# Kernel tuning notes

Measured on AMD Instinct MI355X. Metric: run time of the kernel, lower is better.

Reference implementation:

```python
import jax, jax.numpy as jnp
import numpy as np

B, S, E = 2, 2048, 1024          # batch, seq, emb_size
H, D = 16, 64                     # heads, head_dim
NE, K = 8, 2                      # num_experts, top_k


def setup_inputs() -> dict:
    key = jax.random.key(0)
    ks = jax.random.split(key, 12)
    w = lambda k, shape: jax.random.normal(k, shape, jnp.float32) * 0.02
    return {
        "x": jax.random.normal(ks[0], (B, S, E), jnp.float32),
        "q_w": w(ks[1], (E, E)), "q_b": jnp.zeros((E,), jnp.float32),
        "k_w": w(ks[2], (E, E)), "k_b": jnp.zeros((E,), jnp.float32),
        "v_w": w(ks[3], (E, E)), "v_b": jnp.zeros((E,), jnp.float32),
        "gate_w": w(ks[4], (NE, E)), "gate_b": jnp.zeros((NE,), jnp.float32),
        "expert_w": w(ks[5], (NE, E, E)), "expert_b": jnp.zeros((NE, E), jnp.float32),
        "ffn_w": w(ks[6], (E, E)), "ffn_b": jnp.zeros((E,), jnp.float32),
    }


def _rope_cos_sin(seq_len, dim):
    inv_freq = 1.0 / (10000.0 ** (jnp.arange(0, dim, 2, dtype=jnp.float32) / dim))
    freqs = jnp.outer(jnp.arange(seq_len, dtype=jnp.float32), inv_freq)  # [S, D/2]
    emb = jnp.concatenate([freqs, freqs], axis=-1)                        # [S, D]
    return jnp.cos(emb), jnp.sin(emb)


def _rotate_half(x):
    x1, x2 = jnp.split(x, 2, axis=-1)
    return jnp.concatenate([-x2, x1], axis=-1)


def reference(x, q_w, q_b, k_w, k_b, v_w, v_b, gate_w, gate_b, expert_w, expert_b, ffn_w, ffn_b):
    b, s, _ = x.shape
    q = (x @ q_w.T + q_b).reshape(b, s, H, D)
    k = (x @ k_w.T + k_b).reshape(b, s, H, D)
    v = (x @ v_w.T + v_b).reshape(b, s, H, D)

    cos, sin = _rope_cos_sin(s, D)          # [S, D]
    cos = cos[None, :, None, :]
    sin = sin[None, :, None, :]
    q = q * cos + _rotate_half(q) * sin
    k = k * cos + _rotate_half(k) * sin

    # full (memory-efficient-style) attention, scale 1/sqrt(D)
    scores = jnp.einsum('bqhd,bkhd->bhqk', q, k) / jnp.sqrt(jnp.float32(D))
    attn = jax.nn.softmax(scores, axis=-1)
    attn_out = jnp.einsum('bhqk,bkhd->bqhd', attn, v).reshape(b, s, E)

    # MoE: dense-compute all experts, gather top-k, weighted combine
    gates = jax.nn.softmax(attn_out @ gate_w.T + gate_b, axis=-1)        # [B,S,NE]
    top_gates, top_idx = jax.lax.top_k(gates, K)                          # [B,S,K]
    # Linear per expert: y = x W^T + b,  expert_w: [NE, out, in]
    expert_outputs = jnp.einsum('bsi,noi->bsno', attn_out, expert_w) + expert_b  # [B,S,NE,E]
    sel = jnp.take_along_axis(expert_outputs, top_idx[..., None], axis=2)        # [B,S,K,E]
    moe_out = jnp.einsum('bsk,bskh->bsh', top_gates, sel)                        # [B,S,E]

    # dropout is identity at inference; ffn + residual
    return moe_out @ ffn_w.T + ffn_b + x
```

## Files before the change

### kernel.cpp

```cpp
#include <hip/hip_runtime.h>
#include <hip/hip_bf16.h>

#define B_ 2
#define S_ 2048
#define E_ 1024
#define H_ 16
#define D_ 64
#define NE_ 8
#define TOKENS (B_*S_)
#define QSCALE 0.18033688011112043f

typedef __attribute__((ext_vector_type(8))) short bf16x8;
typedef __attribute__((ext_vector_type(4))) float f32x4;
typedef unsigned short u16;
typedef unsigned int u32;

#if __has_builtin(__builtin_amdgcn_exp2f)
#define EXP2(x) __builtin_amdgcn_exp2f(x)
#else
#define EXP2(x) exp2f(x)
#endif

__device__ __forceinline__ u16 f2bf(float f) {
    u32 u = __float_as_uint(f);
    u32 r = u + 0x7fffu + ((u >> 16) & 1u);
    return (u16)(r >> 16);
}
__device__ __forceinline__ float bf2f(u16 h) {
    return __uint_as_float(((u32)h) << 16);
}
__device__ __forceinline__ void gl2lds16(const void* g, void* l) {
    __builtin_amdgcn_global_load_lds(
        (__attribute__((address_space(1))) void*)(g),
        (__attribute__((address_space(3))) void*)(l), 16, 0, 0);
}
#define MFMA16(a,b,c) __builtin_amdgcn_mfma_f32_16x16x32_bf16(a,b,c,0,0,0)

__global__ void cvt_all_k(
    const float* __restrict__ x,  const float* __restrict__ qw,
    const float* __restrict__ kw, const float* __restrict__ vw,
    const float* __restrict__ fw, const float* __restrict__ ew,
    u16* __restrict__ xh,  u16* __restrict__ qwh, u16* __restrict__ kwh,
    u16* __restrict__ vwh, u16* __restrict__ fwh, u16* __restrict__ ewh,
    float2* __restrict__ tab)
{
    const int blk = blockIdx.x;
    if (blk < 256) {
        const int idx = blk * 256 + threadIdx.x;
        const int s = idx >> 5, d1 = idx & 31;
        const float inv = exp2f(-(float)d1 * 0.41524101186091903f);
        float sn, cs;
        sincosf((float)s * inv, &sn, &cs);
        tab[idx] = make_float2(cs, sn);
        return;
    }
    const int b2 = blk - 256;
    const float* s; u16* d; int off;
    if (b2 < 4096)      { s = x;  d = xh;  off = b2; }
    else if (b2 < 5120) { s = qw; d = qwh; off = b2 - 4096; }
    else if (b2 < 6144) { s = kw; d = kwh; off = b2 - 5120; }
    else if (b2 < 7168) { s = vw; d = vwh; off = b2 - 6144; }
    else if (b2 < 8192) { s = fw; d = fwh; off = b2 - 7168; }
    else                { s = ew; d = ewh; off = b2 - 8192; }
    const size_t i = (size_t)off * 256 + threadIdx.x;
    const float4 v = *(const float4*)(s + i * 4);
    ushort4 H = {f2bf(v.x), f2bf(v.y), f2bf(v.z), f2bf(v.w)};
    *(ushort4*)(d + i * 4) = H;
}

__global__ __launch_bounds__(256,3) void gemm_qkv(
    const u16* __restrict__ Ah,
    const u16* __restrict__ qwh, const u16* __restrict__ kwh,
    const u16* __restrict__ vwh,
    const float* __restrict__ q_b, const float* __restrict__ k_b,
    const float* __restrict__ v_b,
    const float2* __restrict__ tab,
    u16* __restrict__ Qhb, u16* __restrict__ Khb, u16* __restrict__ Vtb)
{
    __shared__ __align__(16) u16 sA[2][128*32], sB[2][128*32];
    const int lin = blockIdx.x + (blockIdx.y << 3) + (blockIdx.z << 8);
    const int n0 = (lin & 7) * 128;
    const int idx = lin >> 3;
    const int z   = idx >> 5;
    const int m0  = (idx & 31) * 128;
    const u16* Bh = (z == 0) ? qwh : (z == 1) ? kwh : vwh;
    const float* bias = (z == 0) ? q_b : (z == 1) ? k_b : v_b;
    const int t = threadIdx.x;
    const int lane = t & 63, w = t >> 6;
    const int wm = w >> 1, wn = w & 1;
    const int lr = lane & 15, qd = lane >> 4;
    f32x4 acc[4][4] = {};
    const size_t gA = (size_t)(m0 + (t >> 2)) * E_ + (t & 3) * 8;
    const size_t gB = (size_t)(n0 + (t >> 2)) * E_ + (t & 3) * 8;
    for (int k0 = 0; k0 < E_; k0 += 64) {
        #pragma unroll
        for (int half = 0; half < 2; half++) {
            #pragma unroll
            for (int is = 0; is < 2; is++) {
                const int ldo = (is * 256 + (t & 192)) * 16;
                const size_t ro = (size_t)is * 64 * E_;
                gl2lds16(Ah + gA + ro + k0 + half*32, (char*)sA[half] + ldo);
                gl2lds16(Bh + gB + ro + k0 + half*32, (char*)sB[half] + ldo);
            }
        }
        __syncthreads();
        #pragma unroll
        for (int half = 0; half < 2; half++) {
            bf16x8 af[4], bfr[4];
            #pragma unroll
            for (int i = 0; i < 4; i++) {
                af[i]  = *(const bf16x8*)&sA[half][(wm*64 + i*16 + lr)*32 + qd*8];
                bfr[i] = *(const bf16x8*)&sB[half][(wn*64 + i*16 + lr)*32 + qd*8];
            }
            #pragma unroll
            for (int i = 0; i < 4; i++)
                #pragma unroll
                for (int j = 0; j < 4; j++)
                    acc[i][j] = MFMA16(af[i], bfr[j], acc[i][j]);
        }
        __syncthreads();
    }
    const int head = (n0 + wn * 64) >> 6;
    if (z < 2) {
        u16* Oh = (z == 0) ? Qhb : Khb;
        const float osc = (z == 0) ? QSCALE : 1.0f;
        #pragma unroll
        for (int j = 0; j < 2; j++) {
            const int d1 = j * 16 + lr;
            const float b1 = bias[head * 64 + d1];
            const float b2 = bias[head * 64 + d1 + 32];
            #pragma unroll
            for (int i = 0; i < 4; i++) {
                #pragma unroll
                for (int r = 0; r < 4; r++) {
                    const int tok = m0 + wm*64 + i*16 + qd*4 + r;
                    const int bb = tok >> 11, ss = tok & (S_ - 1);
                    const float2 t2 = tab[ss * 32 + d1];
                    const float q1 = acc[i][j][r]   + b1;
                    const float q2 = acc[i][j+2][r] + b2;
                    const size_t o = (((size_t)bb * H_ + head) * S_ + ss) * 64 + d1;
                    Oh[o]    = f2bf((q1 * t2.x - q2 * t2.y) * osc);
                    Oh[o+32] = f2bf((q2 * t2.x + q1 * t2.y) * osc);
                }
            }
        }
    } else {
        #pragma unroll
        for (int j = 0; j < 4; j++) {
            const int d = j * 16 + lr;
            const float bv = bias[head * 64 + d];
            #pragma unroll
            for (int i = 0; i < 4; i++)
                #pragma unroll
                for (int r = 0; r < 4; r++) {
                    const int tok = m0 + wm*64 + i*16 + qd*4 + r;
                    const int bb = tok >> 11, ss = tok & (S_ - 1);
                    Vtb[(((size_t)bb * H_ + head) * 64 + d) * S_ + ss] = f2bf(acc[i][j][r] + bv);
                }
        }
    }
}

__global__ __launch_bounds__(256,4) void attn_kernel(
    const u16* __restrict__ Q, const u16* __restrict__ K,
    const u16* __restrict__ Vt,
    float* __restrict__ Opart, float* __restrict__ lpart)
{
    __shared__ __align__(16) u16 sK[2][64*64];
    __shared__ __align__(16) u16 sV[2][64*64];
    __shared__ __align__(16) u16 sP[4][672];
    const int t = threadIdx.x, lane = t & 63, w = t >> 6;
    const int lr = lane & 15, qd = lane >> 4;
    const int lin = blockIdx.x + (blockIdx.y << 4) + (blockIdx.z << 8);
    const int wg  = ((lin & 7) << 7) + (lin >> 3);
    const int q0 = (wg & 15) << 7;
    const int h  = (wg >> 4) & 15;
    const int zc = wg >> 8;
    const int b = zc & 1, sc = zc >> 1;
    const size_t bhS = ((size_t)b * H_ + h) * S_;
    const size_t bhD = ((size_t)b * H_ + h) * 64;
    bf16x8 qf[2][2];
    #pragma unroll
    for (int p = 0; p < 2; p++) {
        const size_t qa = (bhS + q0 + p*64 + w*16 + lr) * 64 + qd * 8;
        qf[p][0] = *(const bf16x8*)&Q[qa];
        qf[p][1] = *(const bf16x8*)&Q[qa + 32];
    }
    bf16x8 vOnes;
    #pragma unroll
    for (int i = 0; i < 8; i++) vOnes[i] = (short)0x3F80;
    f32x4 O[2][4] = {};
    f32x4 Ol[2] = {};

    const int CH0 = w*4 + qd, CH1 = (4 + w)*4 + qd;
    const int sbs0 = CH0 >> 3, doff0 = ((CH0 >> 2) & 1)*32 + (CH0 & 3)*8;
    const int sbs1 = CH1 >> 3, doff1 = ((CH1 >> 2) & 1)*32 + (CH1 & 3)*8;
    auto stage = [&](int bp, int j0) {
        gl2lds16(&K [(bhS + j0 + sbs0*16 + lr)*64 + doff0], (char*)sK[bp] + w*1024);
        gl2lds16(&Vt[(bhD + sbs0*16 + lr)*S_ + j0 + doff0], (char*)sV[bp] + w*1024);
        gl2lds16(&K [(bhS + j0 + sbs1*16 + lr)*64 + doff1], (char*)sK[bp] + (4+w)*1024);
        gl2lds16(&Vt[(bhD + sbs1*16 + lr)*S_ + j0 + doff1], (char*)sV[bp] + (4+w)*1024);
    };

    const int jbeg = sc * 1024;
    stage(0, jbeg);
    for (int jt = 0; jt < 16; ++jt) {
        const int cur = jt & 1;
        asm volatile("s_waitcnt vmcnt(0) lgkmcnt(0)" ::: "memory");
        __builtin_amdgcn_sched_barrier(0);
        __builtin_amdgcn_s_barrier();
        __builtin_amdgcn_sched_barrier(0);
        if (jt + 1 < 16) stage(cur ^ 1, jbeg + (jt + 1) * 64);
        f32x4 Sv[2][4];
        __builtin_amdgcn_s_setprio(1);
        #pragma unroll
        for (int sb = 0; sb < 4; sb++) {
            bf16x8 k0 = *(const bf16x8*)&sK[cur][(sb*8 + qd)*128 + lr*8];
            bf16x8 k1 = *(const bf16x8*)&sK[cur][(sb*8 + 4 + qd)*128 + lr*8];
            f32x4 a0 = {}, a1 = {};
            a0 = MFMA16(k0, qf[0][0], a0);
            a0 = MFMA16(k1, qf[0][1], a0);
            a1 = MFMA16(k0, qf[1][0], a1);
            a1 = MFMA16(k1, qf[1][1], a1);
            Sv[0][sb] = a0;
            Sv[1][sb] = a1;
        }
        __builtin_amdgcn_s_setprio(0);
        uint2 pk[2][4];
        #pragma unroll
        for (int p = 0; p < 2; p++) {
            #pragma unroll
            for (int sb = 0; sb < 4; sb++) {
                const float pv0 = EXP2(Sv[p][sb][0]);
                const float pv1 = EXP2(Sv[p][sb][1]);
                const float pv2 = EXP2(Sv[p][sb][2]);
                const float pv3 = EXP2(Sv[p][sb][3]);
                pk[p][sb].x = __builtin_amdgcn_perm(__float_as_uint(pv1),
                                                    __float_as_uint(pv0), 0x07060302u);
                pk[p][sb].y = __builtin_amdgcn_perm(__float_as_uint(pv3),
                                                    __float_as_uint(pv2), 0x07060302u);
            }
        }
        bf16x8 vv[8];
        #pragma unroll
        for (int ds = 0; ds < 4; ds++) {
            vv[2*ds]   = *(const bf16x8*)&sV[cur][(ds*8 + qd)*128 + lr*8];
            vv[2*ds+1] = *(const bf16x8*)&sV[cur][(ds*8 + 4 + qd)*128 + lr*8];
        }
        #pragma unroll
        for (int p = 0; p < 2; p++) {
            #pragma unroll
            for (int sb = 0; sb < 4; sb++)
                *(uint2*)&sP[w][lr*40 + sb*16 + qd*4] = pk[p][sb];
            bf16x8 p0 = *(const bf16x8*)&sP[w][lr*40 + qd*8];
            bf16x8 p1 = *(const bf16x8*)&sP[w][lr*40 + 32 + qd*8];
            __builtin_amdgcn_s_setprio(1);
            #pragma unroll
            for (int ds = 0; ds < 4; ds++) {
                O[p][ds] = MFMA16(p0, vv[2*ds],   O[p][ds]);
                O[p][ds] = MFMA16(p1, vv[2*ds+1], O[p][ds]);
            }
            Ol[p] = MFMA16(p0, vOnes, Ol[p]);
            Ol[p] = MFMA16(p1, vOnes, Ol[p]);
            __builtin_amdgcn_s_setprio(0);
        }
    }
    float* Op = Opart + (size_t)sc * TOKENS * E_;
    float* lp = lpart + (size_t)sc * TOKENS * H_;
    if (lr == 0) {
        #pragma unroll
        for (int p = 0; p < 2; p++)
            #pragma unroll
            for (int r = 0; r < 4; r++)
                lp[(size_t)(b*S_ + q0 + p*64 + w*16 + qd*4 + r) * H_ + h] = Ol[p][r];
    }
    #pragma unroll
    for (int p = 0; p < 2; p++) {
        const int qb = q0 + p*64 + w*16 + qd*4;
        #pragma unroll
        for (int ds = 0; ds < 4; ds++)
            #pragma unroll
            for (int r = 0; r < 4; r++)
                Op[(size_t)(b*S_ + qb + r) * E_ + h*64 + ds*16 + lr] = O[p][ds][r];
    }
}

__global__ __launch_bounds__(256) void combine_gate(
    const float* __restrict__ Opart, const float* __restrict__ lpart,
    const float* __restrict__ gate_w, const float* __restrict__ gate_b,
    u16* __restrict__ attn_bf, float* __restrict__ gval, int* __restrict__ eidx)
{
    __shared__ float red[4][NE_];
    __shared__ float lg8[NE_];
    const int tok = blockIdx.x;
    const int t = threadIdx.x;
    const int d4 = t * 4;
    const int h = d4 >> 6;
    const float l = lpart[(size_t)tok*H_ + h] + lpart[(size_t)(TOKENS + tok)*H_ + h];
    const float inv = 1.f / l;
    const float4 o1 = *(const float4*)&Opart[(size_t)tok*E_ + d4];
    const float4 o2 = *(const float4*)&Opart[(size_t)(TOKENS + tok)*E_ + d4];
    float v[4] = {(o1.x+o2.x)*inv, (o1.y+o2.y)*inv, (o1.z+o2.z)*inv, (o1.w+o2.w)*inv};
    ushort4 H4 = {f2bf(v[0]), f2bf(v[1]), f2bf(v[2]), f2bf(v[3])};
    *(ushort4*)&attn_bf[(size_t)tok*E_ + d4] = H4;
    float pe[NE_];
    #pragma unroll
    for (int e = 0; e < NE_; e++) {
        const float4 g = *(const float4*)&gate_w[e*E_ + d4];
        pe[e] = v[0]*g.x + v[1]*g.y + v[2]*g.z + v[3]*g.w;
    }
    #pragma unroll
    for (int e = 0; e < NE_; e++) {
        #pragma unroll
        for (int off = 32; off >= 1; off >>= 1)
            pe[e] += __shfl_xor(pe[e], off, 64);
    }
    const int w = t >> 6;
    if ((t & 63) == 0) {
        #pragma unroll
        for (int e = 0; e < NE_; e++) red[w][e] = pe[e];
    }
    __syncthreads();
    if (t < NE_)
        lg8[t] = red[0][t] + red[1][t] + red[2][t] + red[3][t] + gate_b[t];
    __syncthreads();
    if (t == 0) {
        float lg[NE_];
        #pragma unroll
        for (int e = 0; e < NE_; e++) lg[e] = lg8[e];
        float m = lg[0];
        #pragma unroll
        for (int e = 1; e < NE_; e++) m = fmaxf(m, lg[e]);
        float ex[NE_], ssum = 0.f;
        #pragma unroll
        for (int e = 0; e < NE_; e++) { ex[e] = __expf(lg[e]-m); ssum += ex[e]; }
        const float invs = 1.f / ssum;
        int i0 = 0;
        #pragma unroll
        for (int e = 1; e < NE_; e++) if (lg[e] > lg[i0]) i0 = e;
        int i1 = (i0 == 0) ? 1 : 0;
        #pragma unroll
        for (int e = 0; e < NE_; e++) if (e != i0 && lg[e] > lg[i1]) i1 = e;
        eidx[tok*2]     = i0;
        gval[tok*2]     = ex[i0]*invs;
        eidx[tok*2 + 1] = i1;
        gval[tok*2 + 1] = ex[i1]*invs;
    }
}

__global__ __launch_bounds__(256) void build_lists_kernel(
    const int* __restrict__ eidx, int* __restrict__ list, int* __restrict__ counts)
{
    __shared__ int lcnt[NE_], lbase[NE_];
    const int t = threadIdx.x;
    if (t < NE_) lcnt[t] = 0;
    __syncthreads();
    const int ent = blockIdx.x * 512 + t * 2;
    const int e0 = eidx[ent], e1 = eidx[ent + 1];
    const int p0 = atomicAdd(&lcnt[e0], 1);
    const int p1 = atomicAdd(&lcnt[e1], 1);
    __syncthreads();
    if (t < NE_) lbase[t] = atomicAdd(&counts[t], lcnt[t]);
    __syncthreads();
    list[e0 * TOKENS + lbase[e0] + p0] = ent;
    list[e1 * TOKENS + lbase[e1] + p1] = ent + 1;
}

__global__ __launch_bounds__(256,3) void gemm_expert(
    const u16* __restrict__ Abf, const u16* __restrict__ ewh,
    const float* __restrict__ eb, const int* __restrict__ list,
    const int* __restrict__ counts, const float* __restrict__ gval,
    u16* __restrict__ sel)
{
    const int lin = blockIdx.x + (blockIdx.y << 3) + (blockIdx.z << 8);
    const int n0 = (lin & 7) * 128;
    const int idx = lin >> 3;
    const int e   = idx >> 5;
    const int m0  = (idx & 31) * 128;
    const int cnt = counts[e];
    if (m0 >= cnt) return;
    __shared__ __align__(16) u16 sA[2][128*32], sB[2][128*32];
    __shared__ int sEnt[128];
    const int t = threadIdx.x;
    if (t < 128) sEnt[t] = (m0 + t < cnt) ? list[e * TOKENS + m0 + t] : -1;
    __syncthreads();
    const int lane = t & 63, w = t >> 6;
    const int wm = w >> 1, wn = w & 1;
    const int lr = lane & 15, qd = lane >> 4;
    const int e0 = sEnt[t >> 2], e1 = sEnt[64 + (t >> 2)];
    const u16* ga0 = Abf + (size_t)(e0 < 0 ? 0 : (e0 >> 1)) * E_ + (t & 3) * 8;
    const u16* ga1 = Abf + (size_t)(e1 < 0 ? 0 : (e1 >> 1)) * E_ + (t & 3) * 8;
    const u16* gb0 = ewh + (size_t)e * E_ * E_ + (size_t)(n0 + (t >> 2)) * E_ + (t & 3) * 8;
    const u16* gb1 = gb0 + 64 * E_;
    f32x4 acc[4][4] = {};
    for (int k0 = 0; k0 < E_; k0 += 64) {
        #pragma unroll
        for (int half = 0; half < 2; half++) {
            const int l0 = (t & 192) * 16;
            const int l1 = (256 + (t & 192)) * 16;
            const int kk = k0 + half*32;
            gl2lds16(ga0 + kk, (char*)sA[half] + l0);
            gl2lds16(ga1 + kk, (char*)sA[half] + l1);
            gl2lds16(gb0 + kk, (char*)sB[half] + l0);
            gl2lds16(gb1 + kk, (char*)sB[half] + l1);
        }
        __syncthreads();
        #pragma unroll
        for (int half = 0; half < 2; half++) {
            bf16x8 af[4], bfr[4];
            #pragma unroll
            for (int i = 0; i < 4; i++) {
                af[i]  = *(const bf16x8*)&sA[half][(wm*64 + i*16 + lr)*32 + qd*8];
                bfr[i] = *(const bf16x8*)&sB[half][(wn*64 + i*16 + lr)*32 + qd*8];
            }
            #pragma unroll
            for (int i = 0; i < 4; i++)
                #pragma unroll
                for (int j = 0; j < 4; j++)
                    acc[i][j] = MFMA16(af[i], bfr[j], acc[i][j]);
        }
        __syncthreads();
    }
    #pragma unroll
    for (int i = 0; i < 4; i++)
        #pragma unroll
        for (int r = 0; r < 4; r++) {
            const int local = wm*64 + i*16 + qd*4 + r;
            const int ent = sEnt[local];
            if (ent < 0) continue;
            const float g = gval[ent];
            #pragma unroll
            for (int j = 0; j < 4; j++) {
                const int col = n0 + wn*64 + j*16 + lr;
                sel[(size_t)ent * E_ + col] = f2bf((acc[i][j][r] + eb[e * E_ + col]) * g);
            }
        }
}

__global__ void combine_kernel(const u16* __restrict__ sel, u16* __restrict__ moe)
{
    const int g = blockIdx.x * 256 + threadIdx.x;
    const int tok = g >> 8;
    const int c = (g & 255) * 4;
    const u16* a = sel + (size_t)tok * 2048 + c;
    float o[4];
    #pragma unroll
    for (int j = 0; j < 4; j++) o[j] = bf2f(a[j]) + bf2f(a[1024 + j]);
    ushort4 R = {f2bf(o[0]), f2bf(o[1]), f2bf(o[2]), f2bf(o[3])};
    *(ushort4*)(moe + (size_t)tok * E_ + c) = R;
}

__global__ __launch_bounds__(256,2) void gemm_ffn(
    const u16* __restrict__ Ah, const u16* __restrict__ Bh,
    const float* __restrict__ bias, const float* __restrict__ res,
    float* __restrict__ C)
{
    __shared__ __align__(16) u16 sA[2][128*32], sB[2][128*32];
    const int t = threadIdx.x;
    const int lin = blockIdx.x + (blockIdx.y << 3);
    const int n0 = (lin & 7) * 128;
    const int m0 = (lin >> 3) * 128;
    const int lane = t & 63, w = t >> 6;
    const int wm = w >> 1, wn = w & 1;
    const int lr = lane & 15, qd = lane >> 4;
    f32x4 acc[4][4] = {};
    const size_t gA = (size_t)(m0 + (t >> 2)) * E_ + (t & 3) * 8;
    const size_t gB = (size_t)(n0 + (t >> 2)) * E_ + (t & 3) * 8;
    for (int k0 = 0; k0 < E_; k0 += 64) {
        #pragma unroll
        for (int half = 0; half < 2; half++) {
            #pragma unroll
            for (int is = 0; is < 2; is++) {
                const int ldo = (is * 256 + (t & 192)) * 16;
                const size_t ro = (size_t)is * 64 * E_;
                gl2lds16(Ah + gA + ro + k0 + half*32, (char*)sA[half] + ldo);
                gl2lds16(Bh + gB + ro + k0 + half*32, (char*)sB[half] + ldo);
            }
        }
        __syncthreads();
        #pragma unroll
        for (int half = 0; half < 2; half++) {
            bf16x8 af[4], bfr[4];
            #pragma unroll
            for (int i = 0; i < 4; i++) {
                af[i]  = *(const bf16x8*)&sA[half][(wm*64 + i*16 + lr)*32 + qd*8];
                bfr[i] = *(const bf16x8*)&sB[half][(wn*64 + i*16 + lr)*32 + qd*8];
            }
            #pragma unroll
            for (int i = 0; i < 4; i++)
                #pragma unroll
                for (int j = 0; j < 4; j++)
                    acc[i][j] = MFMA16(af[i], bfr[j], acc[i][j]);
        }
        __syncthreads();
    }
    #pragma unroll
    for (int i = 0; i < 4; i++)
        #pragma unroll
        for (int r = 0; r < 4; r++) {
            const int tok = m0 + wm*64 + i*16 + qd*4 + r;
            #pragma unroll
            for (int j = 0; j < 4; j++) {
                const int col = n0 + wn*64 + j*16 + lr;
                C[(size_t)tok * E_ + col] = acc[i][j][r] + bias[col] + res[(size_t)tok * E_ + col];
            }
        }
}

extern "C" void kernel_launch(void* const* d_in, const int* in_sizes, int n_in,
                              void* d_out, int out_size, void* d_ws, size_t ws_size,
                              hipStream_t stream) {
    const float* x      = (const float*)d_in[0];
    const float* q_w    = (const float*)d_in[1];
    const float* q_b    = (const float*)d_in[2];
    const float* k_w    = (const float*)d_in[3];
    const float* k_b    = (const float*)d_in[4];
    const float* v_w    = (const float*)d_in[5];
    const float* v_b    = (const float*)d_in[6];
    const float* gate_w = (const float*)d_in[7];
    const float* gate_b = (const float*)d_in[8];
    const float* ew     = (const float*)d_in[9];
    const float* eb     = (const float*)d_in[10];
    const float* ffn_w  = (const float*)d_in[11];
    const float* ffn_b  = (const float*)d_in[12];
    float* out = (float*)d_out;

    char* p = (char*)d_ws;
    auto alloc = [&](size_t bytes) { char* r = p; p += (bytes + 255) & ~(size_t)255; return r; };
    u16* xh   = (u16*)alloc((size_t)TOKENS*E_*2);
    u16* qwh  = (u16*)alloc((size_t)E_*E_*2);
    u16* kwh  = (u16*)alloc((size_t)E_*E_*2);
    u16* vwh  = (u16*)alloc((size_t)E_*E_*2);
    u16* fwh  = (u16*)alloc((size_t)E_*E_*2);
    u16* ewh  = (u16*)alloc((size_t)NE_*E_*E_*2);
    u16* Qhb  = (u16*)alloc((size_t)TOKENS*E_*2);
    u16* Khb  = (u16*)alloc((size_t)TOKENS*E_*2);
    u16* Vtb  = (u16*)alloc((size_t)TOKENS*E_*2);
    u16* abf  = (u16*)alloc((size_t)TOKENS*E_*2);
    float* Opart = (float*)alloc((size_t)2*TOKENS*E_*4);
    float* lpart = (float*)alloc((size_t)2*TOKENS*H_*4);
    u16* selb = (u16*)alloc((size_t)2*TOKENS*E_*2);
    u16* moeb = (u16*)alloc((size_t)TOKENS*E_*2);
    float2* rtab = (float2*)alloc((size_t)S_*32*8);
    float* gvl = (float*)alloc((size_t)2*TOKENS*4);
    int*   eix = (int*)alloc((size_t)2*TOKENS*4);
    int*   lst = (int*)alloc((size_t)NE_*TOKENS*4);
    int*   cnt = (int*)alloc(256);

    hipMemsetAsync(cnt, 0, 256, stream);

    cvt_all_k<<<16640, 256, 0, stream>>>(x, q_w, k_w, v_w, ffn_w, ew,
                                         xh, qwh, kwh, vwh, fwh, ewh, rtab);

    gemm_qkv<<<dim3(8,32,3), 256, 0, stream>>>(xh, qwh, kwh, vwh,
                                               q_b, k_b, v_b, rtab,
                                               Qhb, Khb, Vtb);

    attn_kernel<<<dim3(16,16,4), 256, 0, stream>>>(Qhb, Khb, Vtb, Opart, lpart);

    combine_gate<<<TOKENS, 256, 0, stream>>>(Opart, lpart, gate_w, gate_b,
                                             abf, gvl, eix);
    build_lists_kernel<<<TOKENS/256, 256, 0, stream>>>(eix, lst, cnt);
    gemm_expert<<<dim3(8,32,8), 256, 0, stream>>>(abf, ewh, eb, lst, cnt, gvl, selb);
    combine_kernel<<<4096, 256, 0, stream>>>(selb, moeb);
    gemm_ffn<<<dim3(8,32), 256, 0, stream>>>(moeb, fwh, ffn_b, x, out);
}
```

Baseline: 293.9 us.

## Fuse expert list building into gating kernel and narrow FFN GEMM tiles

```diff
diff --git a/kernel.cpp b/kernel.cpp
--- a/kernel.cpp
+++ b/kernel.cpp
@@ -288,12 +288,14 @@
 __global__ __launch_bounds__(256) void combine_gate(
     const float* __restrict__ Opart, const float* __restrict__ lpart,
     const float* __restrict__ gate_w, const float* __restrict__ gate_b,
-    u16* __restrict__ attn_bf, float* __restrict__ gval, int* __restrict__ eidx)
+    u16* __restrict__ attn_bf, float* __restrict__ gval,
+    int* __restrict__ list, int* __restrict__ counts)
 {
     __shared__ float red[4][NE_];
     __shared__ float lg8[NE_];
     const int tok = blockIdx.x;
     const int t = threadIdx.x;
+    const int lane = t & 63, w = t >> 6;
     const int d4 = t * 4;
     const int h = d4 >> 6;
     const float l = lpart[(size_t)tok*H_ + h] + lpart[(size_t)(TOKENS + tok)*H_ + h];
@@ -311,15 +313,18 @@
     }
     #pragma unroll
     for (int e = 0; e < NE_; e++) {
-        #pragma unroll
-        for (int off = 32; off >= 1; off >>= 1)
-            pe[e] += __shfl_xor(pe[e], off, 64);
-    }
-    const int w = t >> 6;
-    if ((t & 63) == 0) {
-        #pragma unroll
-        for (int e = 0; e < NE_; e++) red[w][e] = pe[e];
-    }
+        pe[e] += __shfl_xor(pe[e], 32, 64);
+        pe[e] += __shfl_xor(pe[e], 16, 64);
+        pe[e] += __shfl_xor(pe[e], 8, 64);
+    }
+    const int ei = lane >> 3;
+    float x = pe[0];
+    #pragma unroll
+    for (int e = 1; e < NE_; e++) x = (ei == e) ? pe[e] : x;
+    x += __shfl_xor(x, 4, 64);
+    x += __shfl_xor(x, 2, 64);
+    x += __shfl_xor(x, 1, 64);
+    if ((lane & 7) == 0) red[w][ei] = x;
     __syncthreads();
     if (t < NE_)
         lg8[t] = red[0][t] + red[1][t] + red[2][t] + red[3][t] + gate_b[t];
@@ -341,29 +346,13 @@
         int i1 = (i0 == 0) ? 1 : 0;
         #pragma unroll
         for (int e = 0; e < NE_; e++) if (e != i0 && lg[e] > lg[i1]) i1 = e;
-        eidx[tok*2]     = i0;
         gval[tok*2]     = ex[i0]*invs;
-        eidx[tok*2 + 1] = i1;
         gval[tok*2 + 1] = ex[i1]*invs;
-    }
-}
-
-__global__ __launch_bounds__(256) void build_lists_kernel(
-    const int* __restrict__ eidx, int* __restrict__ list, int* __restrict__ counts)
-{
-    __shared__ int lcnt[NE_], lbase[NE_];
-    const int t = threadIdx.x;
-    if (t < NE_) lcnt[t] = 0;
-    __syncthreads();
-    const int ent = blockIdx.x * 512 + t * 2;
-    const int e0 = eidx[ent], e1 = eidx[ent + 1];
-    const int p0 = atomicAdd(&lcnt[e0], 1);
-    const int p1 = atomicAdd(&lcnt[e1], 1);
-    __syncthreads();
-    if (t < NE_) lbase[t] = atomicAdd(&counts[t], lcnt[t]);
-    __syncthreads();
-    list[e0 * TOKENS + lbase[e0] + p0] = ent;
-    list[e1 * TOKENS + lbase[e1] + p1] = ent + 1;
+        const int p0 = atomicAdd(&counts[i0], 1);
+        list[i0 * TOKENS + p0] = tok*2;
+        const int p1 = atomicAdd(&counts[i1], 1);
+        list[i1 * TOKENS + p1] = tok*2 + 1;
+    }
 }
 
 __global__ __launch_bounds__(256,3) void gemm_expert(
@@ -450,46 +439,49 @@
     *(ushort4*)(moe + (size_t)tok * E_ + c) = R;
 }
 
-__global__ __launch_bounds__(256,2) void gemm_ffn(
+__global__ __launch_bounds__(256,3) void gemm_ffn(
     const u16* __restrict__ Ah, const u16* __restrict__ Bh,
     const float* __restrict__ bias, const float* __restrict__ res,
     float* __restrict__ C)
 {
-    __shared__ __align__(16) u16 sA[2][128*32], sB[2][128*32];
+    __shared__ __align__(16) u16 sA[2][128*32], sB[2][64*32];
     const int t = threadIdx.x;
-    const int lin = blockIdx.x + (blockIdx.y << 3);
-    const int n0 = (lin & 7) * 128;
-    const int m0 = (lin >> 3) * 128;
+    const int lin = blockIdx.x + (blockIdx.y << 4);
+    const int idx = lin >> 3;
+    const int m0 = (idx & 31) * 128;
+    const int n0 = ((idx >> 5) * 8 + (lin & 7)) * 64;
     const int lane = t & 63, w = t >> 6;
     const int wm = w >> 1, wn = w & 1;
     const int lr = lane & 15, qd = lane >> 4;
-    f32x4 acc[4][4] = {};
+    f32x4 acc[4][2] = {};
     const size_t gA = (size_t)(m0 + (t >> 2)) * E_ + (t & 3) * 8;
     const size_t gB = (size_t)(n0 + (t >> 2)) * E_ + (t & 3) * 8;
     for (int k0 = 0; k0 < E_; k0 += 64) {
         #pragma unroll
         for (int half = 0; half < 2; half++) {
+            const int kk = k0 + half*32;
             #pragma unroll
             for (int is = 0; is < 2; is++) {
                 const int ldo = (is * 256 + (t & 192)) * 16;
                 const size_t ro = (size_t)is * 64 * E_;
-                gl2lds16(Ah + gA + ro + k0 + half*32, (char*)sA[half] + ldo);
-                gl2lds16(Bh + gB + ro + k0 + half*32, (char*)sB[half] + ldo);
-            }
+                gl2lds16(Ah + gA + ro + kk, (char*)sA[half] + ldo);
+            }
+            gl2lds16(Bh + gB + kk, (char*)sB[half] + t*16);
         }
         __syncthreads();
         #pragma unroll
         for (int half = 0; half < 2; half++) {
-            bf16x8 af[4], bfr[4];
-            #pragma unroll
-            for (int i = 0; i < 4; i++) {
-                af[i]  = *(const bf16x8*)&sA[half][(wm*64 + i*16 + lr)*32 + qd*8];
-                bfr[i] = *(const bf16x8*)&sB[half][(wn*64 + i*16 + lr)*32 + qd*8];
-            }
+            bf16x8 af[4], bfr[2];
+            #pragma unroll
+            for (int i = 0; i < 4; i++)
+                af[i] = *(const bf16x8*)&sA[half][(wm*64 + i*16 + lr)*32 + qd*8];
+            #pragma unroll
+            for (int j = 0; j < 2; j++)
+                bfr[j] = *(const bf16x8*)&sB[half][(wn*32 + j*16 + lr)*32 + qd*8];
             #pragma unroll
             for (int i = 0; i < 4; i++)
                 #pragma unroll
-                for (int j = 0; j < 4; j++)
+                for (int j = 0; j < 2; j++)
                     acc[i][j] = MFMA16(af[i], bfr[j], acc[i][j]);
         }
         __syncthreads();
@@ -500,8 +492,8 @@
         for (int r = 0; r < 4; r++) {
             const int tok = m0 + wm*64 + i*16 + qd*4 + r;
             #pragma unroll
-            for (int j = 0; j < 4; j++) {
-                const int col = n0 + wn*64 + j*16 + lr;
+            for (int j = 0; j < 2; j++) {
+                const int col = n0 + wn*32 + j*16 + lr;
                 C[(size_t)tok * E_ + col] = acc[i][j][r] + bias[col] + res[(size_t)tok * E_ + col];
             }
         }
@@ -543,7 +535,6 @@
     u16* moeb = (u16*)alloc((size_t)TOKENS*E_*2);
     float2* rtab = (float2*)alloc((size_t)S_*32*8);
     float* gvl = (float*)alloc((size_t)2*TOKENS*4);
-    int*   eix = (int*)alloc((size_t)2*TOKENS*4);
     int*   lst = (int*)alloc((size_t)NE_*TOKENS*4);
     int*   cnt = (int*)alloc(256);
 
@@ -559,9 +550,8 @@
     attn_kernel<<<dim3(16,16,4), 256, 0, stream>>>(Qhb, Khb, Vtb, Opart, lpart);
 
     combine_gate<<<TOKENS, 256, 0, stream>>>(Opart, lpart, gate_w, gate_b,
-                                             abf, gvl, eix);
-    build_lists_kernel<<<TOKENS/256, 256, 0, stream>>>(eix, lst, cnt);
+                                             abf, gvl, lst, cnt);
     gemm_expert<<<dim3(8,32,8), 256, 0, stream>>>(abf, ewh, eb, lst, cnt, gvl, selb);
     combine_kernel<<<4096, 256, 0, stream>>>(selb, moeb);
-    gemm_ffn<<<dim3(8,32), 256, 0, stream>>>(moeb, fwh, ffn_b, x, out);
-}
+    gemm_ffn<<<dim3(16,32), 256, 0, stream>>>(moeb, fwh, ffn_b, x, out);
+}
```

Result: slower. 374.5 us (+27.4%).
